# Optimization experiments

Measured on AMD Instinct MI355X. Metric: run time of the kernel, lower is better.

Reference implementation:

```python
import jax, jax.numpy as jnp
import numpy as np

H = 64   # hidden_layers
D = 1    # frame_dimension
N = 2048 # n_samples (batch)
T = 512  # seq_len


def setup_inputs() -> dict:
    key = jax.random.key(0)
    ks = jax.random.split(key, 12)
    s = 1.0 / np.sqrt(H)
    u = lambda k, shape: jax.random.uniform(k, shape, jnp.float32, -s, s)
    return {
        "y": jax.random.normal(ks[0], (N, T), dtype=jnp.float32),
        "W_ih1": u(ks[1], (4 * H, D)),
        "W_hh1": u(ks[2], (4 * H, H)),
        "b_ih1": u(ks[3], (4 * H,)),
        "b_hh1": u(ks[4], (4 * H,)),
        "W_ih2": u(ks[5], (4 * H, H)),
        "W_hh2": u(ks[6], (4 * H, H)),
        "b_ih2": u(ks[7], (4 * H,)),
        "b_hh2": u(ks[8], (4 * H,)),
        "W_lin": u(ks[9], (D, H)),
        "b_lin": u(ks[10], (D,)),
        "pre_output_len": 1,
    }


def _lstm_cell(x, h, c, W_ih, W_hh, b_ih, b_hh):
    # gates in PyTorch LSTMCell order: input, forget, cell(g), output
    g = x @ W_ih.T + b_ih + h @ W_hh.T + b_hh  # [n, 4H]
    i, f, gg, o = jnp.split(g, 4, axis=-1)
    i = jax.nn.sigmoid(i)
    f = jax.nn.sigmoid(f)
    gg = jnp.tanh(gg)
    o = jax.nn.sigmoid(o)
    c2 = f * c + i * gg
    h2 = o * jnp.tanh(c2)
    return h2, c2


def reference(y, W_ih1, W_hh1, b_ih1, b_hh1, W_ih2, W_hh2, b_ih2, b_hh2,
              W_lin, b_lin, pre_output_len):
    n = y.shape[0]
    zeros = jnp.zeros((n, H), dtype=jnp.float32)
    init = (zeros, zeros, zeros, zeros)

    def step(carry, x_t):
        h1, c1, h2, c2 = carry
        h1, c1 = _lstm_cell(x_t, h1, c1, W_ih1, W_hh1, b_ih1, b_hh1)
        h2, c2 = _lstm_cell(h1, h2, c2, W_ih2, W_hh2, b_ih2, b_hh2)
        out = h2 @ W_lin.T + b_lin  # [n, D]
        return (h1, c1, h2, c2), out

    ys = jnp.swapaxes(y, 0, 1)[:, :, None]  # [T, n, 1]
    _, outs = jax.lax.scan(step, init, ys)  # [T, n, D]
    outs = outs[pre_output_len:]            # drop first pre_output_len steps (static)
    # torch.cat along dim=1 of [n, D] chunks -> [n, (T - pre)*D]
    return jnp.transpose(outs, (1, 0, 2)).reshape(n, -1)
```

## Files before the change

### kernel.cpp

```cpp
#include <hip/hip_runtime.h>


typedef __attribute__((ext_vector_type(8))) short short8;
typedef __attribute__((ext_vector_type(4))) float f32x4;

#define NT 512
#define XPITCH 2060
#define XP 0
#define HP 32960
#define RING 51392
#define LDS_BYTES 84160
#define PLANE(layer, buf, hl) (HP + ((((layer) * 2 + (buf)) * 2) + (hl)) * 2304)

__device__ __forceinline__ float fast_rcp(float x) { return __builtin_amdgcn_rcpf(x); }
__device__ __forceinline__ unsigned short bf_rne(float f) {
  unsigned u = __float_as_uint(f);
  return (unsigned short)((u + 0x7FFFu + ((u >> 16) & 1u)) >> 16);
}
__device__ __forceinline__ void split8(const float* p, short8& hi, short8& lo) {
#pragma unroll
  for (int e = 0; e < 8; ++e) {
    float v = p[e];
    unsigned short h = bf_rne(v);
    float hf = __uint_as_float(((unsigned)h) << 16);
    hi[e] = (short)h;
    lo[e] = (short)bf_rne(v - hf);
  }
}
__device__ __forceinline__ unsigned cvt_pk(float a, float b) {
  unsigned r;
  asm("v_cvt_pk_bf16_f32 %0, %1, %2" : "=v"(r) : "v"(a), "v"(b));
  return r;
}
__device__ __forceinline__ f32x4 mfma16(short8 a, short8 b, f32x4 c) {
  return __builtin_amdgcn_mfma_f32_16x16x32_bf16(a, b, c, 0, 0, 0);
}
__device__ __forceinline__ void cell(float i, float f, float gg, float o,
                                     float& c, float& h) {
  const float ei = __expf(-i), ef = __expf(-f), eg = __expf(-2.f * gg),
              eo = __expf(-o);
  const float P = (1.f - eg) * fast_rcp((1.f + ei) * (1.f + eg));
  c = fmaf(c, fast_rcp(1.f + ef), P);
  const float cc = fminf(15.f, fmaxf(-15.f, c));
  const float ec = __expf(-2.f * cc);
  h = (1.f - ec) * fast_rcp((1.f + eo) * (1.f + ec));
}
__device__ __forceinline__ void fast_barrier() {
  __builtin_amdgcn_sched_barrier(0);
  asm volatile("s_waitcnt lgkmcnt(0)" ::: "memory");
  __builtin_amdgcn_s_barrier();
  asm volatile("" ::: "memory");
  __builtin_amdgcn_sched_barrier(0);
}

__global__ __launch_bounds__(512, 2) void lstm2_r10(
    const float* __restrict__ y, const float* __restrict__ Wih1,
    const float* __restrict__ Whh1, const float* __restrict__ bih1,
    const float* __restrict__ bhh1, const float* __restrict__ Wih2,
    const float* __restrict__ Whh2, const float* __restrict__ bih2,
    const float* __restrict__ bhh2, const float* __restrict__ Wlin,
    const float* __restrict__ blin, float* __restrict__ out) {
  extern __shared__ char smem[];
  const int tid = threadIdx.x;
  const int w = tid >> 6;
  const int lane = tid & 63;
  const int g = lane >> 4;
  const int s = lane & 15;
  const int s0 = blockIdx.x * 16;

  for (int i = tid; i < 16 * 512; i += 512) {
    const int ss = i >> 9, t = i & 511;
    *(float*)(smem + XP + ss * XPITCH + t * 4) = y[(size_t)(s0 + ss) * 512 + t];
  }
  for (int i = tid; i < 18432 / 4; i += 512) *(float*)(smem + HP + i * 4) = 0.f;
  const float bl0 = blin[0];
  __syncthreads();

  const int bo0 = s * 144 + 16 * g, bo1 = bo0 + 64;

  if (w < 4) {
    short8 a1h[4][2], a1l[4][2];
#pragma unroll
    for (int p = 0; p < 4; ++p)
#pragma unroll
      for (int c = 0; c < 2; ++c)
        split8(Whh1 + (size_t)(p * 64 + 16 * w + s) * 64 + 32 * c + 8 * g,
               a1h[p][c], a1l[p][c]);
    float bias1c[4][4], wih1c[4][4];
#pragma unroll
    for (int p = 0; p < 4; ++p)
#pragma unroll
      for (int r = 0; r < 4; ++r) {
        const int row = p * 64 + 16 * w + 4 * g + r;
        bias1c[p][r] = bih1[row] + bhh1[row];
        wih1c[p][r] = Wih1[row];
      }
    float c1[4] = {0.f, 0.f, 0.f, 0.f};
    const int hwr0 = s * 144 + 32 * w + 8 * g;
    float xnext = *(const float*)(smem + XP + s * XPITCH);

#pragma unroll 1
    for (int k = 0; k <= NT; ++k) {
      if (k >= 65 && (k & 63) == 1) {
        const int thr = w * 64 + lane;
        const int s2 = thr >> 4, iq = thr & 15;
        const int f0 = k - 67;
        float* ob = out + (size_t)(s0 + s2) * 511;
#pragma unroll
        for (int u = 0; u < 4; ++u) {
          const int p = f0 + iq * 4 + u;
          if (p >= 0) {
            const char* op = smem + RING + (p & 127) * 256 + s2 * 4;
            ob[p] = *(const float*)(op) + *(const float*)(op + 64) +
                    *(const float*)(op + 128) + *(const float*)(op + 192) + bl0;
          }
        }
      }
      if (k < NT) {
        const float x = xnext;
        const int nk = (k + 1 < NT) ? k + 1 : NT - 1;
        xnext = *(const float*)(smem + XP + s * XPITCH + nk * 4);
        const int rp0 = PLANE(0, (k - 1) & 1, 0), rp1 = PLANE(0, (k - 1) & 1, 1);
        const short8 Bh0 = *(const short8*)(smem + rp0 + bo0);
        const short8 Bl0 = *(const short8*)(smem + rp1 + bo0);
        const short8 Bh1 = *(const short8*)(smem + rp0 + bo1);
        const short8 Bl1 = *(const short8*)(smem + rp1 + bo1);
        f32x4 acc[4], acx[4];
#pragma unroll
        for (int p = 0; p < 4; ++p) {
#pragma unroll
          for (int r = 0; r < 4; ++r) acc[p][r] = fmaf(wih1c[p][r], x, bias1c[p][r]);
          acx[p] = (f32x4){0.f, 0.f, 0.f, 0.f};
        }
        __builtin_amdgcn_s_setprio(1);
#pragma unroll
        for (int p = 0; p < 4; ++p) acc[p] = mfma16(a1h[p][0], Bh0, acc[p]);
#pragma unroll
        for (int p = 0; p < 4; ++p) acx[p] = mfma16(a1h[p][1], Bh1, acx[p]);
#pragma unroll
        for (int p = 0; p < 4; ++p) acc[p] = mfma16(a1h[p][0], Bl0, acc[p]);
#pragma unroll
        for (int p = 0; p < 4; ++p) acx[p] = mfma16(a1h[p][1], Bl1, acx[p]);
#pragma unroll
        for (int p = 0; p < 4; ++p) acc[p] = mfma16(a1l[p][0], Bh0, acc[p]);
#pragma unroll
        for (int p = 0; p < 4; ++p) acx[p] = mfma16(a1l[p][1], Bh1, acx[p]);
        __builtin_amdgcn_s_setprio(0);
#pragma unroll
        for (int p = 0; p < 4; ++p) acc[p] += acx[p];

        float h1n[4];
#pragma unroll
        for (int r = 0; r < 4; ++r)
          cell(acc[0][r], acc[1][r], acc[2][r], acc[3][r], c1[r], h1n[r]);
        const unsigned hA = cvt_pk(h1n[0], h1n[1]), hB = cvt_pk(h1n[2], h1n[3]);
        const unsigned lA = cvt_pk(h1n[0] - __uint_as_float(hA << 16),
                                   h1n[1] - __uint_as_float(hA & 0xFFFF0000u));
        const unsigned lB = cvt_pk(h1n[2] - __uint_as_float(hB << 16),
                                   h1n[3] - __uint_as_float(hB & 0xFFFF0000u));
        *(uint2*)(smem + PLANE(0, k & 1, 0) + hwr0) = make_uint2(hA, hB);
        *(uint2*)(smem + PLANE(0, k & 1, 1) + hwr0) = make_uint2(lA, lB);
      }
      fast_barrier();
    }
    __syncthreads();
    {
      const int thr = w * 64 + lane;
      for (int e = thr; e < 65 * 16; e += 256) {
        const int s2 = e & 15, off = e >> 4;
        const int p = 446 + off;
        const char* op = smem + RING + (p & 127) * 256 + s2 * 4;
        out[(size_t)(s0 + s2) * 511 + p] =
            *(const float*)(op) + *(const float*)(op + 64) +
            *(const float*)(op + 128) + *(const float*)(op + 192) + bl0;
      }
    }
  } else {
    const int ow = w - 4;
    short8 a2h[4][4], a2l[4][4];
#pragma unroll
    for (int p = 0; p < 4; ++p)
#pragma unroll
      for (int c = 0; c < 4; ++c) {
        const float* src = (c < 2) ? (Wih2 + (size_t)(p * 64 + 16 * ow + s) * 64 + 32 * c + 8 * g)
                                   : (Whh2 + (size_t)(p * 64 + 16 * ow + s) * 64 + 32 * (c - 2) + 8 * g);
        split8(src, a2h[p][c], a2l[p][c]);
      }
    float bias2c[4][4], wlinc[4];
#pragma unroll
    for (int p = 0; p < 4; ++p)
#pragma unroll
      for (int r = 0; r < 4; ++r)
        bias2c[p][r] = bih2[p * 64 + 16 * ow + 4 * g + r] +
                       bhh2[p * 64 + 16 * ow + 4 * g + r];
#pragma unroll
    for (int r = 0; r < 4; ++r) wlinc[r] = Wlin[16 * ow + 4 * g + r];
    float c2[4] = {0.f, 0.f, 0.f, 0.f};
    float h2p[4] = {0.f, 0.f, 0.f, 0.f};
    const int hwr0 = s * 144 + 32 * ow + 8 * g;

#pragma unroll 1
    for (int k = 0; k <= NT; ++k) {
      if (k >= 3) {
        float pw = wlinc[0] * h2p[0];
        pw = fmaf(wlinc[1], h2p[1], pw);
        pw = fmaf(wlinc[2], h2p[2], pw);
        pw = fmaf(wlinc[3], h2p[3], pw);
        pw += __shfl_xor(pw, 16, 64);
        pw += __shfl_xor(pw, 32, 64);
        if (g == 0)
          *(float*)(smem + RING + ((k - 3) & 127) * 256 + ow * 64 + s * 4) = pw;
      }
      if (k >= 1) {
        const int rp0 = PLANE(0, (k - 1) & 1, 0), rp1 = PLANE(0, (k - 1) & 1, 1);
        const int rq0 = PLANE(1, k & 1, 0), rq1 = PLANE(1, k & 1, 1);
        const short8 Bh0 = *(const short8*)(smem + rp0 + bo0);
        const short8 Bl0 = *(const short8*)(smem + rp1 + bo0);
        const short8 Bh1 = *(const short8*)(smem + rp0 + bo1);
        const short8 Bl1 = *(const short8*)(smem + rp1 + bo1);
        const short8 Ch0 = *(const short8*)(smem + rq0 + bo0);
        const short8 Cl0 = *(const short8*)(smem + rq1 + bo0);
        const short8 Ch1 = *(const short8*)(smem + rq0 + bo1);
        const short8 Cl1 = *(const short8*)(smem + rq1 + bo1);
        f32x4 acc[4], acx[4];
#pragma unroll
        for (int p = 0; p < 4; ++p) {
          acc[p] = (f32x4){bias2c[p][0], bias2c[p][1], bias2c[p][2], bias2c[p][3]};
          acx[p] = (f32x4){0.f, 0.f, 0.f, 0.f};
        }
        __builtin_amdgcn_s_setprio(1);
#pragma unroll
        for (int p = 0; p < 4; ++p) acc[p] = mfma16(a2h[p][0], Bh0, acc[p]);
#pragma unroll
        for (int p = 0; p < 4; ++p) acx[p] = mfma16(a2h[p][1], Bh1, acx[p]);
#pragma unroll
        for (int p = 0; p < 4; ++p) acc[p] = mfma16(a2h[p][0], Bl0, acc[p]);
#pragma unroll
        for (int p = 0; p < 4; ++p) acx[p] = mfma16(a2h[p][1], Bl1, acx[p]);
#pragma unroll
        for (int p = 0; p < 4; ++p) acc[p] = mfma16(a2l[p][0], Bh0, acc[p]);
#pragma unroll
        for (int p = 0; p < 4; ++p) acx[p] = mfma16(a2l[p][1], Bh1, acx[p]);
#pragma unroll
        for (int p = 0; p < 4; ++p) acc[p] = mfma16(a2h[p][2], Ch0, acc[p]);
#pragma unroll
        for (int p = 0; p < 4; ++p) acx[p] = mfma16(a2h[p][3], Ch1, acx[p]);
#pragma unroll
        for (int p = 0; p < 4; ++p) acc[p] = mfma16(a2h[p][2], Cl0, acc[p]);
#pragma unroll
        for (int p = 0; p < 4; ++p) acx[p] = mfma16(a2h[p][3], Cl1, acx[p]);
#pragma unroll
        for (int p = 0; p < 4; ++p) acc[p] = mfma16(a2l[p][2], Ch0, acc[p]);
#pragma unroll
        for (int p = 0; p < 4; ++p) acx[p] = mfma16(a2l[p][3], Ch1, acx[p]);
        __builtin_amdgcn_s_setprio(0);
#pragma unroll
        for (int p = 0; p < 4; ++p) acc[p] += acx[p];

        float h2n[4];
#pragma unroll
        for (int r = 0; r < 4; ++r)
          cell(acc[0][r], acc[1][r], acc[2][r], acc[3][r], c2[r], h2n[r]);
        const unsigned hA = cvt_pk(h2n[0], h2n[1]), hB = cvt_pk(h2n[2], h2n[3]);
        const unsigned lA = cvt_pk(h2n[0] - __uint_as_float(hA << 16),
                                   h2n[1] - __uint_as_float(hA & 0xFFFF0000u));
        const unsigned lB = cvt_pk(h2n[2] - __uint_as_float(hB << 16),
                                   h2n[3] - __uint_as_float(hB & 0xFFFF0000u));
        *(uint2*)(smem + PLANE(1, (k - 1) & 1, 0) + hwr0) = make_uint2(hA, hB);
        *(uint2*)(smem + PLANE(1, (k - 1) & 1, 1) + hwr0) = make_uint2(lA, lB);
#pragma unroll
        for (int r = 0; r < 4; ++r) h2p[r] = h2n[r];
      }
      fast_barrier();
    }
    {
      float pw = wlinc[0] * h2p[0];
      pw = fmaf(wlinc[1], h2p[1], pw);
      pw = fmaf(wlinc[2], h2p[2], pw);
      pw = fmaf(wlinc[3], h2p[3], pw);
      pw += __shfl_xor(pw, 16, 64);
      pw += __shfl_xor(pw, 32, 64);
      if (g == 0)
        *(float*)(smem + RING + (510 & 127) * 256 + ow * 64 + s * 4) = pw;
    }
    __syncthreads();
  }
}

extern "C" void kernel_launch(void* const* d_in, const int* in_sizes, int n_in,
                              void* d_out, int out_size, void* d_ws, size_t ws_size,
                              hipStream_t stream) {
  const float* y    = (const float*)d_in[0];
  const float* Wih1 = (const float*)d_in[1];
  const float* Whh1 = (const float*)d_in[2];
  const float* bih1 = (const float*)d_in[3];
  const float* bhh1 = (const float*)d_in[4];
  const float* Wih2 = (const float*)d_in[5];
  const float* Whh2 = (const float*)d_in[6];
  const float* bih2 = (const float*)d_in[7];
  const float* bhh2 = (const float*)d_in[8];
  const float* Wlin = (const float*)d_in[9];
  const float* blin = (const float*)d_in[10];
  float* out = (float*)d_out;

  hipFuncSetAttribute((const void*)lstm2_r10,
                      hipFuncAttributeMaxDynamicSharedMemorySize, LDS_BYTES);
  lstm2_r10<<<dim3(128), dim3(512), LDS_BYTES, stream>>>(
      y, Wih1, Whh1, bih1, bhh1, Wih2, Whh2, bih2, bhh2, Wlin, blin, out);
}
```

Baseline: 649.6 us.

## Split each timestep into two barrier phases so layer-1 cell math overlaps layer-2 MFMAs

Each step now has two half-steps, each ending in a barrier. Layer-1 waves issue their MFMAs, hit a barrier, then run the gate nonlinearities and write h1. Layer-2 waves run their cell math from the previous MFMA results in the first phase and their MFMAs in the second. The goal is for one wave group's transcendental work to overlap the other group's matrix work instead of both finishing each step in lockstep. It doubles the barrier count per timestep and shifts the output-ring flush indices, which adds sync overhead and some off-by-one risk.

```diff
diff --git a/kernel.cpp b/kernel.cpp
--- a/kernel.cpp
+++ b/kernel.cpp
@@ -53,7 +53,7 @@
   __builtin_amdgcn_sched_barrier(0);
 }
 
-__global__ __launch_bounds__(512, 2) void lstm2_r10(
+__global__ __launch_bounds__(512, 2) void lstm2_r11(
     const float* __restrict__ y, const float* __restrict__ Wih1,
     const float* __restrict__ Whh1, const float* __restrict__ bih1,
     const float* __restrict__ bhh1, const float* __restrict__ Wih2,
@@ -98,34 +98,32 @@
     float c1[4] = {0.f, 0.f, 0.f, 0.f};
     const int hwr0 = s * 144 + 32 * w + 8 * g;
     float xnext = *(const float*)(smem + XP + s * XPITCH);
+    f32x4 acc[4], acx[4];
 
 #pragma unroll 1
-    for (int k = 0; k <= NT; ++k) {
-      if (k >= 65 && (k & 63) == 1) {
+    for (int m = 0; m <= NT + 1; ++m) {
+      if (m >= 68 && (m & 63) == 4) {
         const int thr = w * 64 + lane;
         const int s2 = thr >> 4, iq = thr & 15;
-        const int f0 = k - 67;
+        const int f0 = m - 68;
         float* ob = out + (size_t)(s0 + s2) * 511;
 #pragma unroll
         for (int u = 0; u < 4; ++u) {
           const int p = f0 + iq * 4 + u;
-          if (p >= 0) {
-            const char* op = smem + RING + (p & 127) * 256 + s2 * 4;
-            ob[p] = *(const float*)(op) + *(const float*)(op + 64) +
-                    *(const float*)(op + 128) + *(const float*)(op + 192) + bl0;
-          }
-        }
-      }
-      if (k < NT) {
+          const char* op = smem + RING + (p & 127) * 256 + s2 * 4;
+          ob[p] = *(const float*)(op) + *(const float*)(op + 64) +
+                  *(const float*)(op + 128) + *(const float*)(op + 192) + bl0;
+        }
+      }
+      if (m < NT) {
         const float x = xnext;
-        const int nk = (k + 1 < NT) ? k + 1 : NT - 1;
+        const int nk = (m + 1 < NT) ? m + 1 : NT - 1;
         xnext = *(const float*)(smem + XP + s * XPITCH + nk * 4);
-        const int rp0 = PLANE(0, (k - 1) & 1, 0), rp1 = PLANE(0, (k - 1) & 1, 1);
+        const int rp0 = PLANE(0, (m - 1) & 1, 0), rp1 = PLANE(0, (m - 1) & 1, 1);
         const short8 Bh0 = *(const short8*)(smem + rp0 + bo0);
         const short8 Bl0 = *(const short8*)(smem + rp1 + bo0);
         const short8 Bh1 = *(const short8*)(smem + rp0 + bo1);
         const short8 Bl1 = *(const short8*)(smem + rp1 + bo1);
-        f32x4 acc[4], acx[4];
 #pragma unroll
         for (int p = 0; p < 4; ++p) {
 #pragma unroll
@@ -146,9 +144,11 @@
 #pragma unroll
         for (int p = 0; p < 4; ++p) acx[p] = mfma16(a1l[p][1], Bh1, acx[p]);
         __builtin_amdgcn_s_setprio(0);
+      }
+      fast_barrier();
+      if (m < NT) {
 #pragma unroll
         for (int p = 0; p < 4; ++p) acc[p] += acx[p];
-
         float h1n[4];
 #pragma unroll
         for (int r = 0; r < 4; ++r)
@@ -158,17 +158,17 @@
                                    h1n[1] - __uint_as_float(hA & 0xFFFF0000u));
         const unsigned lB = cvt_pk(h1n[2] - __uint_as_float(hB << 16),
                                    h1n[3] - __uint_as_float(hB & 0xFFFF0000u));
-        *(uint2*)(smem + PLANE(0, k & 1, 0) + hwr0) = make_uint2(hA, hB);
-        *(uint2*)(smem + PLANE(0, k & 1, 1) + hwr0) = make_uint2(lA, lB);
+        *(uint2*)(smem + PLANE(0, m & 1, 0) + hwr0) = make_uint2(hA, hB);
+        *(uint2*)(smem + PLANE(0, m & 1, 1) + hwr0) = make_uint2(lA, lB);
       }
       fast_barrier();
     }
     __syncthreads();
     {
       const int thr = w * 64 + lane;
-      for (int e = thr; e < 65 * 16; e += 256) {
+      for (int e = thr; e < 63 * 16; e += 256) {
         const int s2 = e & 15, off = e >> 4;
-        const int p = 446 + off;
+        const int p = 448 + off;
         const char* op = smem + RING + (p & 127) * 256 + s2 * 4;
         out[(size_t)(s0 + s2) * 511 + p] =
             *(const float*)(op) + *(const float*)(op + 64) +
@@ -196,24 +196,40 @@
 #pragma unroll
     for (int r = 0; r < 4; ++r) wlinc[r] = Wlin[16 * ow + 4 * g + r];
     float c2[4] = {0.f, 0.f, 0.f, 0.f};
-    float h2p[4] = {0.f, 0.f, 0.f, 0.f};
     const int hwr0 = s * 144 + 32 * ow + 8 * g;
+    f32x4 acc[4], acx[4];
 
 #pragma unroll 1
-    for (int k = 0; k <= NT; ++k) {
-      if (k >= 3) {
-        float pw = wlinc[0] * h2p[0];
-        pw = fmaf(wlinc[1], h2p[1], pw);
-        pw = fmaf(wlinc[2], h2p[2], pw);
-        pw = fmaf(wlinc[3], h2p[3], pw);
-        pw += __shfl_xor(pw, 16, 64);
-        pw += __shfl_xor(pw, 32, 64);
-        if (g == 0)
-          *(float*)(smem + RING + ((k - 3) & 127) * 256 + ow * 64 + s * 4) = pw;
-      }
-      if (k >= 1) {
-        const int rp0 = PLANE(0, (k - 1) & 1, 0), rp1 = PLANE(0, (k - 1) & 1, 1);
-        const int rq0 = PLANE(1, k & 1, 0), rq1 = PLANE(1, k & 1, 1);
+    for (int m = 0; m <= NT + 1; ++m) {
+      if (m >= 2) {
+#pragma unroll
+        for (int p = 0; p < 4; ++p) acc[p] += acx[p];
+        float h2n[4];
+#pragma unroll
+        for (int r = 0; r < 4; ++r)
+          cell(acc[0][r], acc[1][r], acc[2][r], acc[3][r], c2[r], h2n[r]);
+        const unsigned hA = cvt_pk(h2n[0], h2n[1]), hB = cvt_pk(h2n[2], h2n[3]);
+        const unsigned lA = cvt_pk(h2n[0] - __uint_as_float(hA << 16),
+                                   h2n[1] - __uint_as_float(hA & 0xFFFF0000u));
+        const unsigned lB = cvt_pk(h2n[2] - __uint_as_float(hB << 16),
+                                   h2n[3] - __uint_as_float(hB & 0xFFFF0000u));
+        *(uint2*)(smem + PLANE(1, m & 1, 0) + hwr0) = make_uint2(hA, hB);
+        *(uint2*)(smem + PLANE(1, m & 1, 1) + hwr0) = make_uint2(lA, lB);
+        if (m >= 3) {
+          float pw = wlinc[0] * h2n[0];
+          pw = fmaf(wlinc[1], h2n[1], pw);
+          pw = fmaf(wlinc[2], h2n[2], pw);
+          pw = fmaf(wlinc[3], h2n[3], pw);
+          pw += __shfl_xor(pw, 16, 64);
+          pw += __shfl_xor(pw, 32, 64);
+          if (g == 0)
+            *(float*)(smem + RING + ((m - 3) & 127) * 256 + ow * 64 + s * 4) = pw;
+        }
+      }
+      fast_barrier();
+      if (m >= 1 && m <= NT) {
+        const int rp0 = PLANE(0, (m - 1) & 1, 0), rp1 = PLANE(0, (m - 1) & 1, 1);
+        const int rq0 = PLANE(1, m & 1, 0), rq1 = PLANE(1, m & 1, 1);
         const short8 Bh0 = *(const short8*)(smem + rp0 + bo0);
         const short8 Bl0 = *(const short8*)(smem + rp1 + bo0);
         const short8 Bh1 = *(const short8*)(smem + rp0 + bo1);
@@ -222,7 +238,6 @@
         const short8 Cl0 = *(const short8*)(smem + rq1 + bo0);
         const short8 Ch1 = *(const short8*)(smem + rq0 + bo1);
         const short8 Cl1 = *(const short8*)(smem + rq1 + bo1);
-        f32x4 acc[4], acx[4];
 #pragma unroll
         for (int p = 0; p < 4; ++p) {
           acc[p] = (f32x4){bias2c[p][0], bias2c[p][1], bias2c[p][2], bias2c[p][3]};
@@ -254,34 +269,8 @@
 #pragma unroll
         for (int p = 0; p < 4; ++p) acx[p] = mfma16(a2l[p][3], Ch1, acx[p]);
         __builtin_amdgcn_s_setprio(0);
-#pragma unroll
-        for (int p = 0; p < 4; ++p) acc[p] += acx[p];
-
-        float h2n[4];
-#pragma unroll
-        for (int r = 0; r < 4; ++r)
-          cell(acc[0][r], acc[1][r], acc[2][r], acc[3][r], c2[r], h2n[r]);
-        const unsigned hA = cvt_pk(h2n[0], h2n[1]), hB = cvt_pk(h2n[2], h2n[3]);
-        const unsigned lA = cvt_pk(h2n[0] - __uint_as_float(hA << 16),
-                                   h2n[1] - __uint_as_float(hA & 0xFFFF0000u));
-        const unsigned lB = cvt_pk(h2n[2] - __uint_as_float(hB << 16),
-                                   h2n[3] - __uint_as_float(hB & 0xFFFF0000u));
-        *(uint2*)(smem + PLANE(1, (k - 1) & 1, 0) + hwr0) = make_uint2(hA, hB);
-        *(uint2*)(smem + PLANE(1, (k - 1) & 1, 1) + hwr0) = make_uint2(lA, lB);
-#pragma unroll
-        for (int r = 0; r < 4; ++r) h2p[r] = h2n[r];
-      }
-      fast_barrier();
-    }
-    {
-      float pw = wlinc[0] * h2p[0];
-      pw = fmaf(wlinc[1], h2p[1], pw);
-      pw = fmaf(wlinc[2], h2p[2], pw);
-      pw = fmaf(wlinc[3], h2p[3], pw);
-      pw += __shfl_xor(pw, 16, 64);
-      pw += __shfl_xor(pw, 32, 64);
-      if (g == 0)
-        *(float*)(smem + RING + (510 & 127) * 256 + ow * 64 + s * 4) = pw;
+      }
+      fast_barrier();
     }
     __syncthreads();
   }
@@ -303,8 +292,8 @@
   const float* blin = (const float*)d_in[10];
   float* out = (float*)d_out;
 
-  hipFuncSetAttribute((const void*)lstm2_r10,
+  hipFuncSetAttribute((const void*)lstm2_r11,
                       hipFuncAttributeMaxDynamicSharedMemorySize, LDS_BYTES);
-  lstm2_r10<<<dim3(128), dim3(512), LDS_BYTES, stream>>>(
+  lstm2_r11<<<dim3(128), dim3(512), LDS_BYTES, stream>>>(
       y, Wih1, Whh1, bih1, bhh1, Wih2, Whh2, bih2, bhh2, Wlin, blin, out);
 }
```

After: 728.1 us. 1.12x slower.
